# Optimization experiments

Hardware: AMD Instinct MI355X
Metric: run time of the kernel (lower is better)

The kernel has to match this reference:

```python
import jax, jax.numpy as jnp
import numpy as np

N_NODES = 100000
N_EDGES = 300000
D = 256
N_LAYERS = 4
BN_EPS = 1e-5


def setup_inputs() -> dict:
    key = jax.random.key(0)
    ks = jax.random.split(key, 6)
    x = jax.random.normal(ks[0], (N_NODES, D), dtype=jnp.float32)
    rows = jax.random.randint(ks[1], (N_EDGES,), 0, N_NODES)
    cols = jax.random.randint(ks[2], (N_EDGES,), 0, N_NODES)
    vals = jax.random.uniform(ks[3], (N_EDGES,), dtype=jnp.float32)
    stdv = 1.0 / np.sqrt(D).astype(np.float32)
    weights = jax.random.uniform(ks[4], (N_LAYERS, D, D), jnp.float32, -stdv, stdv)
    self_weights = jax.random.uniform(ks[5], (N_LAYERS, D, D), jnp.float32, -stdv, stdv)
    gammas = jnp.ones((N_LAYERS, D), jnp.float32)
    betas = jnp.zeros((N_LAYERS, D), jnp.float32)
    return {"x": x, "vals": vals, "weights": weights, "self_weights": self_weights,
            "gammas": gammas, "betas": betas, "rows": rows, "cols": cols}


def reference(x, vals, weights, self_weights, gammas, betas, rows, cols):
    n = x.shape[0]

    def gcn_layer(h, W, SW, gamma, beta):
        # support = h @ W  -> dense [N, D]
        support = h @ W
        # spmm(adj, support): out[i] = sum_{e: rows[e]==i} vals[e] * support[cols[e]]
        agg = jax.ops.segment_sum(vals[:, None] * support[cols], rows, num_segments=n)
        out = agg + h @ SW  # self-loop term (withloop=True)
        # BatchNorm1d over nodes (training-mode batch stats, biased variance)
        mean = out.mean(axis=0)
        var = out.var(axis=0)
        out = gamma * (out - mean) * jax.lax.rsqrt(var + BN_EPS) + beta
        return jax.nn.relu(out)

    h = x
    for i in range(N_LAYERS):
        h = gcn_layer(h, weights[i], self_weights[i], gammas[i], betas[i])
    # aggrmethod='concat', dense=False -> cat(final, input)
    return jnp.concatenate([h, x], axis=1)
```

## Files before the change

### kernel.cpp

```cpp
#include <hip/hip_runtime.h>
#include <hip/hip_bf16.h>
#include <stdint.h>

#define M_NODES 100000
#define NE      300000
#define D       256
#define D2      512
#define NLAYERS 4

typedef float  f32x4  __attribute__((ext_vector_type(4)));
typedef __bf16 bf16x8 __attribute__((ext_vector_type(8)));

static __device__ __forceinline__ float bf2f(uint32_t u) {
  union { uint32_t i; float f; } v; v.i = u << 16; return v.f;
}
static __device__ __forceinline__ uint32_t f2bf(float f) {
  union { float f; uint32_t i; } v; v.f = f;
  return (v.i + 0x7fffu + ((v.i >> 16) & 1u)) >> 16;
}
static __device__ __forceinline__ void gload_lds16(const void* g, void* l) {
  __builtin_amdgcn_global_load_lds((const __attribute__((address_space(1))) uint32_t*)g,
                                   (__attribute__((address_space(3))) uint32_t*)l, 16, 0, 0);
}

__global__ void hist_kernel(const int* __restrict__ rows, int* __restrict__ counts) {
  int e = blockIdx.x * 256 + threadIdx.x;
  if (e < NE) atomicAdd(&counts[rows[e]], 1);
}

__global__ void scan1_kernel(const int* __restrict__ counts, int* __restrict__ rp,
                             int* __restrict__ bsum) {
  __shared__ int sd[256];
  int tid = threadIdx.x;
  int base = blockIdx.x * 1024 + tid * 4;
  int v0 = (base + 0 < M_NODES) ? counts[base + 0] : 0;
  int v1 = (base + 1 < M_NODES) ? counts[base + 1] : 0;
  int v2 = (base + 2 < M_NODES) ? counts[base + 2] : 0;
  int v3 = (base + 3 < M_NODES) ? counts[base + 3] : 0;
  int tsum = v0 + v1 + v2 + v3;
  sd[tid] = tsum; __syncthreads();
  for (int off = 1; off < 256; off <<= 1) {
    int x = sd[tid];
    if (tid >= off) x += sd[tid - off];
    __syncthreads(); sd[tid] = x; __syncthreads();
  }
  int excl = sd[tid] - tsum;
  if (base + 0 < M_NODES) rp[base + 0] = excl; excl += v0;
  if (base + 1 < M_NODES) rp[base + 1] = excl; excl += v1;
  if (base + 2 < M_NODES) rp[base + 2] = excl; excl += v2;
  if (base + 3 < M_NODES) rp[base + 3] = excl;
  if (tid == 255) bsum[blockIdx.x] = sd[255];
}

__global__ void scan2_kernel(const int* __restrict__ bsum, int* __restrict__ boff) {
  __shared__ int sd[128];
  int tid = threadIdx.x;
  int v = (tid < 98) ? bsum[tid] : 0;
  sd[tid] = v; __syncthreads();
  for (int off = 1; off < 128; off <<= 1) {
    int x = sd[tid];
    if (tid >= off) x += sd[tid - off];
    __syncthreads(); sd[tid] = x; __syncthreads();
  }
  if (tid < 98) boff[tid] = sd[tid] - v;
}

__global__ void scan3_kernel(int* __restrict__ rp, const int* __restrict__ boff,
                             int* __restrict__ cursor) {
  int i = blockIdx.x * 256 + threadIdx.x;
  if (i > M_NODES) return;
  int v = (i < M_NODES) ? rp[i] + boff[i >> 10] : NE;
  rp[i] = v;
  if (i < M_NODES) cursor[i] = v;
}

__global__ void scatter_kernel(const int* __restrict__ rows, const int* __restrict__ cols,
                               const float* __restrict__ vals, int* __restrict__ cursor,
                               int* __restrict__ e_col, float* __restrict__ e_val) {
  int e = blockIdx.x * 256 + threadIdx.x;
  if (e >= NE) return;
  int r = rows[e];
  int p = atomicAdd(&cursor[r], 1);
  e_col[p] = cols[e];
  e_val[p] = vals[e];
}

__global__ void conv_x_kernel(const float* __restrict__ x, ushort* __restrict__ h) {
  size_t idx = (size_t)blockIdx.x * 256 + threadIdx.x;
  size_t i = idx >> 6; int c = (int)(idx & 63) * 4;
  float4 v = *(const float4*)(x + i * D + c);
  ushort4 o;
  o.x = (ushort)f2bf(v.x); o.y = (ushort)f2bf(v.y);
  o.z = (ushort)f2bf(v.z); o.w = (ushort)f2bf(v.w);
  *(ushort4*)(h + i * D + c) = o;
}

__global__ void copy_x_kernel(const float* __restrict__ x, float* __restrict__ out) {
  size_t idx = (size_t)blockIdx.x * 256 + threadIdx.x;
  size_t i = idx >> 6; int c = (int)(idx & 63) * 4;
  float4 v = *(const float4*)(x + i * D + c);
  *(float4*)(out + i * D2 + D + c) = v;
}

__global__ void conv_w_kernel(const float* __restrict__ W, const float* __restrict__ SW,
                              ushort* __restrict__ Bt) {
  int idx = blockIdx.x * 256 + threadIdx.x;
  if (idx >= NLAYERS * D2 * D) return;
  int k = idx & (D - 1);
  int n = (idx >> 8) & (D2 - 1);
  int layer = idx >> 17;
  float v = (n < D) ? W[(size_t)layer * D * D + k * D + n]
                    : SW[(size_t)layer * D * D + k * D + (n - D)];
  Bt[idx] = (ushort)f2bf(v);
}

#define BM 128
#define BN 128
#define BK 64

__global__ __launch_bounds__(256, 2)
void gemm_kernel(const ushort* __restrict__ h, const ushort* __restrict__ Bt,
                 ushort* __restrict__ outAB) {
  __shared__ __align__(16) ushort As[BM * BK];
  __shared__ __align__(16) ushort Bs[BN * BK];
  const int tid = threadIdx.x;
  const int m0 = blockIdx.x * BM;
  const int n0 = blockIdx.y * BN;
  const int wv = tid >> 6, l = tid & 63;
  const int wr = wv >> 1, wc = wv & 1;
  const int lrow = l & 15, lhi = l >> 4;

  f32x4 acc[4][4] = {};

  const int arow = tid >> 3;
  const int acb  = (tid & 7) << 4;

#pragma unroll
  for (int s = 0; s < 4; ++s) {
    const int k0 = s * BK;
#pragma unroll
    for (int p = 0; p < 4; ++p) {
      int row = p * 32 + arow;
      int grow = m0 + row; if (grow >= M_NODES) grow = M_NODES - 1;
      int gcb = acb ^ ((row & 7) << 4);
      gload_lds16(h + (size_t)grow * D + k0 + (gcb >> 1), As + row * BK + (acb >> 1));
    }
#pragma unroll
    for (int p = 0; p < 4; ++p) {
      int row = p * 32 + arow;
      int gn = n0 + row;
      int gcb = acb ^ ((row & 7) << 4);
      gload_lds16(Bt + (size_t)gn * D + k0 + (gcb >> 1), Bs + row * BK + (acb >> 1));
    }
    __syncthreads();
#pragma unroll
    for (int kk = 0; kk < 2; ++kk) {
      bf16x8 af[4], bfr[4];
#pragma unroll
      for (int mi = 0; mi < 4; ++mi) {
        int row = wr * 64 + mi * 16 + lrow;
        int off = row * 128 + ((kk * 64 + lhi * 16) ^ ((row & 7) << 4));
        af[mi] = *(const bf16x8*)((const char*)As + off);
      }
#pragma unroll
      for (int nj = 0; nj < 4; ++nj) {
        int row = wc * 64 + nj * 16 + lrow;
        int off = row * 128 + ((kk * 64 + lhi * 16) ^ ((row & 7) << 4));
        bfr[nj] = *(const bf16x8*)((const char*)Bs + off);
      }
#pragma unroll
      for (int mi = 0; mi < 4; ++mi)
#pragma unroll
        for (int nj = 0; nj < 4; ++nj)
          acc[mi][nj] = __builtin_amdgcn_mfma_f32_16x16x32_bf16(af[mi], bfr[nj], acc[mi][nj], 0, 0, 0);
    }
    __syncthreads();
  }

#pragma unroll
  for (int mi = 0; mi < 4; ++mi) {
#pragma unroll
    for (int nj = 0; nj < 4; ++nj) {
      int gc = n0 + wc * 64 + nj * 16 + lrow;
#pragma unroll
      for (int r = 0; r < 4; ++r) {
        int grow = m0 + wr * 64 + mi * 16 + lhi * 4 + r;
        if (grow < M_NODES)
          outAB[(size_t)grow * D2 + gc] = (ushort)f2bf(acc[mi][nj][r]);
      }
    }
  }
}

#define SPMM_CHUNK 16

__global__ __launch_bounds__(256, 4)
void spmm_kernel(ushort* __restrict__ AB, const int* __restrict__ rp,
                 const int* __restrict__ e_col, const float* __restrict__ e_val,
                 float* __restrict__ stats) {
  __shared__ float sstats[2 * D];
  for (int i = threadIdx.x; i < 2 * D; i += 256) sstats[i] = 0.f;
  __syncthreads();

  const int wv = threadIdx.x >> 6, l = threadIdx.x & 63;
  const int wave = blockIdx.x * 4 + wv;
  const int row0 = wave * SPMM_CHUNK;

  float s0 = 0, s1 = 0, s2 = 0, s3 = 0, q0 = 0, q1 = 0, q2 = 0, q3 = 0;

  if (row0 < M_NODES) {
    const int nrows = (M_NODES - row0 < SPMM_CHUNK) ? (M_NODES - row0) : SPMM_CHUNK;
    int myrp = (l <= nrows) ? rp[row0 + l] : 0;

    for (int t = 0; t < nrows; ++t) {
      const int i = row0 + t;
      const int e0 = __shfl(myrp, t);
      const int e1 = __shfl(myrp, t + 1);
      const int deg = e1 - e0;

      const ushort4 st = *(const ushort4*)(AB + (size_t)i * D2 + D + 4 * l);
      float a0 = bf2f(st.x), a1 = bf2f(st.y), a2 = bf2f(st.z), a3 = bf2f(st.w);

      for (int b = 0; b < deg; b += 64) {
        const int nb = (deg - b < 64) ? (deg - b) : 64;
        int   myc = (l < nb) ? e_col[e0 + b + l] : 0;
        float myv = (l < nb) ? e_val[e0 + b + l] : 0.f;

        for (int e = 0; e < nb; e += 4) {
          int cc[4]; float vv[4]; ushort4 sp[4];
#pragma unroll
          for (int j = 0; j < 4; ++j) {
            int ee = (e + j < nb) ? (e + j) : (nb - 1);
            cc[j] = __shfl(myc, ee);
            vv[j] = (e + j < nb) ? __shfl(myv, e + j) : 0.f;
            sp[j] = *(const ushort4*)(AB + (size_t)cc[j] * D2 + 4 * l);
          }
#pragma unroll
          for (int j = 0; j < 4; ++j) {
            a0 += vv[j] * bf2f(sp[j].x);
            a1 += vv[j] * bf2f(sp[j].y);
            a2 += vv[j] * bf2f(sp[j].z);
            a3 += vv[j] * bf2f(sp[j].w);
          }
        }
      }

      ushort4 o;
      o.x = (ushort)f2bf(a0); o.y = (ushort)f2bf(a1);
      o.z = (ushort)f2bf(a2); o.w = (ushort)f2bf(a3);
      *(ushort4*)(AB + (size_t)i * D2 + D + 4 * l) = o;
      s0 += a0; q0 += a0 * a0; s1 += a1; q1 += a1 * a1;
      s2 += a2; q2 += a2 * a2; s3 += a3; q3 += a3 * a3;
    }
  }

  const int c0 = 4 * l;
  atomicAdd(&sstats[c0 + 0], s0); atomicAdd(&sstats[c0 + 1], s1);
  atomicAdd(&sstats[c0 + 2], s2); atomicAdd(&sstats[c0 + 3], s3);
  atomicAdd(&sstats[D + c0 + 0], q0); atomicAdd(&sstats[D + c0 + 1], q1);
  atomicAdd(&sstats[D + c0 + 2], q2); atomicAdd(&sstats[D + c0 + 3], q3);
  __syncthreads();
  atomicAdd(&stats[threadIdx.x], sstats[threadIdx.x]);
  atomicAdd(&stats[D + threadIdx.x], sstats[D + threadIdx.x]);
}

__global__ void bn_fin_kernel(const float* __restrict__ stats, const float* __restrict__ gamma,
                              const float* __restrict__ beta, float* __restrict__ scale,
                              float* __restrict__ shift) {
  int c = threadIdx.x;
  float mean = stats[c] * (1.0f / M_NODES);
  float var = stats[D + c] * (1.0f / M_NODES) - mean * mean;
  float rstd = rsqrtf(var + 1e-5f);
  float sc = gamma[c] * rstd;
  scale[c] = sc;
  shift[c] = beta[c] - mean * sc;
}

__global__ void norm_bf16_kernel(const ushort* __restrict__ AB, const float* __restrict__ scale,
                                 const float* __restrict__ shift, ushort* __restrict__ hout) {
  size_t idx = (size_t)blockIdx.x * 256 + threadIdx.x;
  if (idx >= (size_t)M_NODES * D / 8) return;
  size_t i = idx >> 5; int c = (int)(idx & 31) * 8;
  uint4 u = *(const uint4*)(AB + i * D2 + D + c);
  float4 sc0 = *(const float4*)(scale + c), sc1 = *(const float4*)(scale + c + 4);
  float4 sh0 = *(const float4*)(shift + c), sh1 = *(const float4*)(shift + c + 4);
  float f0 = fmaxf(bf2f(u.x & 0xffff) * sc0.x + sh0.x, 0.f);
  float f1 = fmaxf(bf2f(u.x >> 16)    * sc0.y + sh0.y, 0.f);
  float f2 = fmaxf(bf2f(u.y & 0xffff) * sc0.z + sh0.z, 0.f);
  float f3 = fmaxf(bf2f(u.y >> 16)    * sc0.w + sh0.w, 0.f);
  float f4 = fmaxf(bf2f(u.z & 0xffff) * sc1.x + sh1.x, 0.f);
  float f5 = fmaxf(bf2f(u.z >> 16)    * sc1.y + sh1.y, 0.f);
  float f6 = fmaxf(bf2f(u.w & 0xffff) * sc1.z + sh1.z, 0.f);
  float f7 = fmaxf(bf2f(u.w >> 16)    * sc1.w + sh1.w, 0.f);
  uint4 o;
  o.x = f2bf(f0) | (f2bf(f1) << 16);
  o.y = f2bf(f2) | (f2bf(f3) << 16);
  o.z = f2bf(f4) | (f2bf(f5) << 16);
  o.w = f2bf(f6) | (f2bf(f7) << 16);
  *(uint4*)(hout + i * D + c) = o;
}

__global__ void norm_f32_out_kernel(const ushort* __restrict__ AB, const float* __restrict__ scale,
                                    const float* __restrict__ shift, float* __restrict__ out) {
  size_t idx = (size_t)blockIdx.x * 256 + threadIdx.x;
  if (idx >= (size_t)M_NODES * D / 8) return;
  size_t i = idx >> 5; int c = (int)(idx & 31) * 8;
  uint4 u = *(const uint4*)(AB + i * D2 + D + c);
  float4 sc0 = *(const float4*)(scale + c), sc1 = *(const float4*)(scale + c + 4);
  float4 sh0 = *(const float4*)(shift + c), sh1 = *(const float4*)(shift + c + 4);
  float4 r0, r1;
  r0.x = fmaxf(bf2f(u.x & 0xffff) * sc0.x + sh0.x, 0.f);
  r0.y = fmaxf(bf2f(u.x >> 16)    * sc0.y + sh0.y, 0.f);
  r0.z = fmaxf(bf2f(u.y & 0xffff) * sc0.z + sh0.z, 0.f);
  r0.w = fmaxf(bf2f(u.y >> 16)    * sc0.w + sh0.w, 0.f);
  r1.x = fmaxf(bf2f(u.z & 0xffff) * sc1.x + sh1.x, 0.f);
  r1.y = fmaxf(bf2f(u.z >> 16)    * sc1.y + sh1.y, 0.f);
  r1.z = fmaxf(bf2f(u.w & 0xffff) * sc1.z + sh1.z, 0.f);
  r1.w = fmaxf(bf2f(u.w >> 16)    * sc1.w + sh1.w, 0.f);
  *(float4*)(out + i * D2 + c) = r0;
  *(float4*)(out + i * D2 + c + 4) = r1;
}

extern "C" void kernel_launch(void* const* d_in, const int* in_sizes, int n_in,
                              void* d_out, int out_size, void* d_ws, size_t ws_size,
                              hipStream_t stream) {
  const float* x      = (const float*)d_in[0];
  const float* vals   = (const float*)d_in[1];
  const float* W      = (const float*)d_in[2];
  const float* SW     = (const float*)d_in[3];
  const float* gammas = (const float*)d_in[4];
  const float* betas  = (const float*)d_in[5];
  const int*   rows   = (const int*)d_in[6];
  const int*   cols   = (const int*)d_in[7];
  float* out = (float*)d_out;

  char* ws = (char*)d_ws;
  size_t off = 0;
  auto alloc = [&](size_t bytes) {
    void* p = ws + off;
    off = (off + bytes + 255) & ~(size_t)255;
    return p;
  };
  ushort* h    = (ushort*)alloc((size_t)M_NODES * D * 2);
  ushort* AB   = (ushort*)alloc((size_t)M_NODES * D2 * 2);
  ushort* Bt   = (ushort*)alloc((size_t)NLAYERS * D2 * D * 2);
  int*   rp    = (int*)alloc((M_NODES + 1) * 4);
  int*   cursor= (int*)alloc((M_NODES + 1) * 4);
  int*   e_col = (int*)alloc(NE * 4);
  float* e_val = (float*)alloc(NE * 4);
  int*   bsum  = (int*)alloc(512);
  int*   boff  = (int*)alloc(512);
  float* stats = (float*)alloc(NLAYERS * 2 * D * 4);
  float* scale = (float*)alloc(D * 4);
  float* shift = (float*)alloc(D * 4);

  hipMemsetAsync(cursor, 0, (size_t)M_NODES * 4, stream);
  hipMemsetAsync(stats, 0, (size_t)NLAYERS * 2 * D * 4, stream);

  hist_kernel<<<(NE + 255) / 256, 256, 0, stream>>>(rows, cursor);
  scan1_kernel<<<98, 256, 0, stream>>>(cursor, rp, bsum);
  scan2_kernel<<<1, 128, 0, stream>>>(bsum, boff);
  scan3_kernel<<<(M_NODES + 256) / 256, 256, 0, stream>>>(rp, boff, cursor);
  scatter_kernel<<<(NE + 255) / 256, 256, 0, stream>>>(rows, cols, vals, cursor, e_col, e_val);

  conv_x_kernel<<<(M_NODES * D / 4) / 256, 256, 0, stream>>>(x, h);
  conv_w_kernel<<<(NLAYERS * D2 * D) / 256, 256, 0, stream>>>(W, SW, Bt);
  copy_x_kernel<<<(M_NODES * D / 4) / 256, 256, 0, stream>>>(x, out);

  const int spmm_blocks = (M_NODES + SPMM_CHUNK * 4 - 1) / (SPMM_CHUNK * 4);
  for (int lyr = 0; lyr < NLAYERS; ++lyr) {
    gemm_kernel<<<dim3((M_NODES + BM - 1) / BM, D2 / BN), 256, 0, stream>>>(
        h, Bt + (size_t)lyr * D2 * D, AB);
    spmm_kernel<<<spmm_blocks, 256, 0, stream>>>(AB, rp, e_col, e_val,
                                                 stats + (size_t)lyr * 2 * D);
    bn_fin_kernel<<<1, 256, 0, stream>>>(stats + (size_t)lyr * 2 * D, gammas + lyr * D,
                                         betas + lyr * D, scale, shift);
    if (lyr < NLAYERS - 1)
      norm_bf16_kernel<<<(M_NODES * D / 8) / 256 + 1, 256, 0, stream>>>(AB, scale, shift, h);
    else
      norm_f32_out_kernel<<<(M_NODES * D / 8) / 256 + 1, 256, 0, stream>>>(AB, scale, shift, out);
  }
}
```

Baseline: 708.6 us.

## Restructure SpMM to half-wave rows with preloaded edges; fuse BN finalize into norm

The SpMM kernel now has each half-wave handle one row with 8 columns per lane and 16-byte gathers, processing two rows at once. The column and value lists for the whole 16-row chunk are preloaded into registers and broadcast with shuffles, falling back to global loads past 128 edges. The separate BN finalize kernel is folded into the normalization kernel, which recomputes scale and shift per thread, and the x-to-bf16 conversion and output copy of x are merged into one kernel. This cuts kernel launches and per-edge load latency, at the cost of divergence when the two rows paired in a wave differ in degree.

```diff
diff --git a/kernel.cpp b/kernel.cpp
--- a/kernel.cpp
+++ b/kernel.cpp
@@ -85,21 +85,16 @@
   e_val[p] = vals[e];
 }
 
-__global__ void conv_x_kernel(const float* __restrict__ x, ushort* __restrict__ h) {
+__global__ void prep_x_kernel(const float* __restrict__ x, ushort* __restrict__ h,
+                              float* __restrict__ out) {
   size_t idx = (size_t)blockIdx.x * 256 + threadIdx.x;
   size_t i = idx >> 6; int c = (int)(idx & 63) * 4;
   float4 v = *(const float4*)(x + i * D + c);
+  *(float4*)(out + i * D2 + D + c) = v;
   ushort4 o;
   o.x = (ushort)f2bf(v.x); o.y = (ushort)f2bf(v.y);
   o.z = (ushort)f2bf(v.z); o.w = (ushort)f2bf(v.w);
   *(ushort4*)(h + i * D + c) = o;
-}
-
-__global__ void copy_x_kernel(const float* __restrict__ x, float* __restrict__ out) {
-  size_t idx = (size_t)blockIdx.x * 256 + threadIdx.x;
-  size_t i = idx >> 6; int c = (int)(idx & 63) * 4;
-  float4 v = *(const float4*)(x + i * D + c);
-  *(float4*)(out + i * D2 + D + c) = v;
 }
 
 __global__ void conv_w_kernel(const float* __restrict__ W, const float* __restrict__ SW,
@@ -203,122 +198,141 @@
   __syncthreads();
 
   const int wv = threadIdx.x >> 6, l = threadIdx.x & 63;
+  const int hl = l >> 5, lc = l & 31;
   const int wave = blockIdx.x * 4 + wv;
   const int row0 = wave * SPMM_CHUNK;
 
-  float s0 = 0, s1 = 0, s2 = 0, s3 = 0, q0 = 0, q1 = 0, q2 = 0, q3 = 0;
+  float s[8] = {}, q[8] = {};
 
   if (row0 < M_NODES) {
-    const int nrows = (M_NODES - row0 < SPMM_CHUNK) ? (M_NODES - row0) : SPMM_CHUNK;
-    int myrp = (l <= nrows) ? rp[row0 + l] : 0;
-
-    for (int t = 0; t < nrows; ++t) {
-      const int i = row0 + t;
-      const int e0 = __shfl(myrp, t);
-      const int e1 = __shfl(myrp, t + 1);
-      const int deg = e1 - e0;
-
-      const ushort4 st = *(const ushort4*)(AB + (size_t)i * D2 + D + 4 * l);
-      float a0 = bf2f(st.x), a1 = bf2f(st.y), a2 = bf2f(st.z), a3 = bf2f(st.w);
-
-      for (int b = 0; b < deg; b += 64) {
-        const int nb = (deg - b < 64) ? (deg - b) : 64;
-        int   myc = (l < nb) ? e_col[e0 + b + l] : 0;
-        float myv = (l < nb) ? e_val[e0 + b + l] : 0.f;
-
-        for (int e = 0; e < nb; e += 4) {
-          int cc[4]; float vv[4]; ushort4 sp[4];
-#pragma unroll
-          for (int j = 0; j < 4; ++j) {
-            int ee = (e + j < nb) ? (e + j) : (nb - 1);
-            cc[j] = __shfl(myc, ee);
-            vv[j] = (e + j < nb) ? __shfl(myv, e + j) : 0.f;
-            sp[j] = *(const ushort4*)(AB + (size_t)cc[j] * D2 + 4 * l);
+    int myrp = (l <= SPMM_CHUNK) ? rp[row0 + l] : 0;
+    const int ebase = __shfl(myrp, 0);
+    const int ecnt  = __shfl(myrp, SPMM_CHUNK) - ebase;
+    int   myc0 = (l < ecnt)      ? e_col[ebase + l]      : 0;
+    float myv0 = (l < ecnt)      ? e_val[ebase + l]      : 0.f;
+    int   myc1 = (64 + l < ecnt) ? e_col[ebase + 64 + l] : 0;
+    float myv1 = (64 + l < ecnt) ? e_val[ebase + 64 + l] : 0.f;
+
+    for (int t = 0; t < SPMM_CHUNK; t += 2) {
+      const int i = row0 + t + hl;
+      const int eA0 = __shfl(myrp, t);
+      const int eA1 = __shfl(myrp, t + 1);
+      const int eB1 = __shfl(myrp, t + 2);
+      const int d0 = eA1 - eA0, d1 = eB1 - eA1;
+      const int e0  = hl ? eA1 : eA0;
+      const int deg = hl ? d1  : d0;
+      const int degmax = (d0 > d1) ? d0 : d1;
+
+      float a[8] = {};
+
+      for (int b = 0; b < degmax; b += 4) {
+        float vv[4]; uint4 sp[4];
+#pragma unroll
+        for (int j = 0; j < 4; ++j) {
+          int ej = b + j;
+          int ecl = (ej < deg) ? ej : ((deg > 0) ? deg - 1 : 0);
+          int slot = e0 - ebase + ecl;
+          int sl = slot & 63;
+          int cA = __shfl(myc0, sl);
+          int cB = __shfl(myc1, sl);
+          float vA = __shfl(myv0, sl);
+          float vB = __shfl(myv1, sl);
+          int   c = (slot < 64) ? cA : cB;
+          float v = (slot < 64) ? vA : vB;
+          if (slot >= 128 && ej < deg) {
+            c = e_col[e0 + ecl]; v = e_val[e0 + ecl];
           }
-#pragma unroll
-          for (int j = 0; j < 4; ++j) {
-            a0 += vv[j] * bf2f(sp[j].x);
-            a1 += vv[j] * bf2f(sp[j].y);
-            a2 += vv[j] * bf2f(sp[j].z);
-            a3 += vv[j] * bf2f(sp[j].w);
-          }
+          vv[j] = (ej < deg) ? v : 0.f;
+          sp[j] = *(const uint4*)(AB + (size_t)c * D2 + lc * 8);
+        }
+#pragma unroll
+        for (int j = 0; j < 4; ++j) {
+          a[0] += vv[j] * bf2f(sp[j].x & 0xffff);
+          a[1] += vv[j] * bf2f(sp[j].x >> 16);
+          a[2] += vv[j] * bf2f(sp[j].y & 0xffff);
+          a[3] += vv[j] * bf2f(sp[j].y >> 16);
+          a[4] += vv[j] * bf2f(sp[j].z & 0xffff);
+          a[5] += vv[j] * bf2f(sp[j].z >> 16);
+          a[6] += vv[j] * bf2f(sp[j].w & 0xffff);
+          a[7] += vv[j] * bf2f(sp[j].w >> 16);
         }
       }
 
-      ushort4 o;
-      o.x = (ushort)f2bf(a0); o.y = (ushort)f2bf(a1);
-      o.z = (ushort)f2bf(a2); o.w = (ushort)f2bf(a3);
-      *(ushort4*)(AB + (size_t)i * D2 + D + 4 * l) = o;
-      s0 += a0; q0 += a0 * a0; s1 += a1; q1 += a1 * a1;
-      s2 += a2; q2 += a2 * a2; s3 += a3; q3 += a3 * a3;
-    }
-  }
-
-  const int c0 = 4 * l;
-  atomicAdd(&sstats[c0 + 0], s0); atomicAdd(&sstats[c0 + 1], s1);
-  atomicAdd(&sstats[c0 + 2], s2); atomicAdd(&sstats[c0 + 3], s3);
-  atomicAdd(&sstats[D + c0 + 0], q0); atomicAdd(&sstats[D + c0 + 1], q1);
-  atomicAdd(&sstats[D + c0 + 2], q2); atomicAdd(&sstats[D + c0 + 3], q3);
+      const uint4 st = *(const uint4*)(AB + (size_t)i * D2 + D + lc * 8);
+      a[0] += bf2f(st.x & 0xffff); a[1] += bf2f(st.x >> 16);
+      a[2] += bf2f(st.y & 0xffff); a[3] += bf2f(st.y >> 16);
+      a[4] += bf2f(st.z & 0xffff); a[5] += bf2f(st.z >> 16);
+      a[6] += bf2f(st.w & 0xffff); a[7] += bf2f(st.w >> 16);
+
+      uint4 o;
+      o.x = f2bf(a[0]) | (f2bf(a[1]) << 16);
+      o.y = f2bf(a[2]) | (f2bf(a[3]) << 16);
+      o.z = f2bf(a[4]) | (f2bf(a[5]) << 16);
+      o.w = f2bf(a[6]) | (f2bf(a[7]) << 16);
+      *(uint4*)(AB + (size_t)i * D2 + D + lc * 8) = o;
+
+#pragma unroll
+      for (int k = 0; k < 8; ++k) { s[k] += a[k]; q[k] += a[k] * a[k]; }
+    }
+  }
+
+  const int c0 = lc * 8;
+#pragma unroll
+  for (int k = 0; k < 8; ++k) {
+    atomicAdd(&sstats[c0 + k], s[k]);
+    atomicAdd(&sstats[D + c0 + k], q[k]);
+  }
   __syncthreads();
   atomicAdd(&stats[threadIdx.x], sstats[threadIdx.x]);
   atomicAdd(&stats[D + threadIdx.x], sstats[D + threadIdx.x]);
 }
 
-__global__ void bn_fin_kernel(const float* __restrict__ stats, const float* __restrict__ gamma,
-                              const float* __restrict__ beta, float* __restrict__ scale,
-                              float* __restrict__ shift) {
-  int c = threadIdx.x;
-  float mean = stats[c] * (1.0f / M_NODES);
-  float var = stats[D + c] * (1.0f / M_NODES) - mean * mean;
-  float rstd = rsqrtf(var + 1e-5f);
-  float sc = gamma[c] * rstd;
-  scale[c] = sc;
-  shift[c] = beta[c] - mean * sc;
-}
-
-__global__ void norm_bf16_kernel(const ushort* __restrict__ AB, const float* __restrict__ scale,
-                                 const float* __restrict__ shift, ushort* __restrict__ hout) {
-  size_t idx = (size_t)blockIdx.x * 256 + threadIdx.x;
-  if (idx >= (size_t)M_NODES * D / 8) return;
-  size_t i = idx >> 5; int c = (int)(idx & 31) * 8;
-  uint4 u = *(const uint4*)(AB + i * D2 + D + c);
-  float4 sc0 = *(const float4*)(scale + c), sc1 = *(const float4*)(scale + c + 4);
-  float4 sh0 = *(const float4*)(shift + c), sh1 = *(const float4*)(shift + c + 4);
-  float f0 = fmaxf(bf2f(u.x & 0xffff) * sc0.x + sh0.x, 0.f);
-  float f1 = fmaxf(bf2f(u.x >> 16)    * sc0.y + sh0.y, 0.f);
-  float f2 = fmaxf(bf2f(u.y & 0xffff) * sc0.z + sh0.z, 0.f);
-  float f3 = fmaxf(bf2f(u.y >> 16)    * sc0.w + sh0.w, 0.f);
-  float f4 = fmaxf(bf2f(u.z & 0xffff) * sc1.x + sh1.x, 0.f);
-  float f5 = fmaxf(bf2f(u.z >> 16)    * sc1.y + sh1.y, 0.f);
-  float f6 = fmaxf(bf2f(u.w & 0xffff) * sc1.z + sh1.z, 0.f);
-  float f7 = fmaxf(bf2f(u.w >> 16)    * sc1.w + sh1.w, 0.f);
-  uint4 o;
-  o.x = f2bf(f0) | (f2bf(f1) << 16);
-  o.y = f2bf(f2) | (f2bf(f3) << 16);
-  o.z = f2bf(f4) | (f2bf(f5) << 16);
-  o.w = f2bf(f6) | (f2bf(f7) << 16);
-  *(uint4*)(hout + i * D + c) = o;
-}
-
-__global__ void norm_f32_out_kernel(const ushort* __restrict__ AB, const float* __restrict__ scale,
-                                    const float* __restrict__ shift, float* __restrict__ out) {
-  size_t idx = (size_t)blockIdx.x * 256 + threadIdx.x;
-  if (idx >= (size_t)M_NODES * D / 8) return;
-  size_t i = idx >> 5; int c = (int)(idx & 31) * 8;
-  uint4 u = *(const uint4*)(AB + i * D2 + D + c);
-  float4 sc0 = *(const float4*)(scale + c), sc1 = *(const float4*)(scale + c + 4);
-  float4 sh0 = *(const float4*)(shift + c), sh1 = *(const float4*)(shift + c + 4);
-  float4 r0, r1;
-  r0.x = fmaxf(bf2f(u.x & 0xffff) * sc0.x + sh0.x, 0.f);
-  r0.y = fmaxf(bf2f(u.x >> 16)    * sc0.y + sh0.y, 0.f);
-  r0.z = fmaxf(bf2f(u.y & 0xffff) * sc0.z + sh0.z, 0.f);
-  r0.w = fmaxf(bf2f(u.y >> 16)    * sc0.w + sh0.w, 0.f);
-  r1.x = fmaxf(bf2f(u.z & 0xffff) * sc1.x + sh1.x, 0.f);
-  r1.y = fmaxf(bf2f(u.z >> 16)    * sc1.y + sh1.y, 0.f);
-  r1.z = fmaxf(bf2f(u.w & 0xffff) * sc1.z + sh1.z, 0.f);
-  r1.w = fmaxf(bf2f(u.w >> 16)    * sc1.w + sh1.w, 0.f);
-  *(float4*)(out + i * D2 + c) = r0;
-  *(float4*)(out + i * D2 + c + 4) = r1;
+template<bool LAST>
+__global__ void norm_kernel(const ushort* __restrict__ AB, const float* __restrict__ stats,
+                            const float* __restrict__ gamma, const float* __restrict__ beta,
+                            ushort* __restrict__ hout, float* __restrict__ out) {
+  const int cs = threadIdx.x & 31;
+  const int rr = threadIdx.x >> 5;
+  const int c0 = cs * 8;
+
+  float sc[8], sh[8];
+#pragma unroll
+  for (int k = 0; k < 8; ++k) {
+    float mean = stats[c0 + k] * (1.0f / M_NODES);
+    float var  = stats[D + c0 + k] * (1.0f / M_NODES) - mean * mean;
+    float rstd = rsqrtf(var + 1e-5f);
+    float g = gamma[c0 + k];
+    sc[k] = g * rstd;
+    sh[k] = beta[c0 + k] - mean * sc[k];
+  }
+
+  const int r0 = blockIdx.x * 64;
+#pragma unroll
+  for (int rb = 0; rb < 8; ++rb) {
+    int r = r0 + rb * 8 + rr;
+    if (r >= M_NODES) break;
+    const uint4 u = *(const uint4*)(AB + (size_t)r * D2 + D + c0);
+    float f[8];
+    f[0] = bf2f(u.x & 0xffff); f[1] = bf2f(u.x >> 16);
+    f[2] = bf2f(u.y & 0xffff); f[3] = bf2f(u.y >> 16);
+    f[4] = bf2f(u.z & 0xffff); f[5] = bf2f(u.z >> 16);
+    f[6] = bf2f(u.w & 0xffff); f[7] = bf2f(u.w >> 16);
+#pragma unroll
+    for (int k = 0; k < 8; ++k) f[k] = fmaxf(f[k] * sc[k] + sh[k], 0.f);
+    if (LAST) {
+      float4 r0v = { f[0], f[1], f[2], f[3] };
+      float4 r1v = { f[4], f[5], f[6], f[7] };
+      *(float4*)(out + (size_t)r * D2 + c0) = r0v;
+      *(float4*)(out + (size_t)r * D2 + c0 + 4) = r1v;
+    } else {
+      uint4 o;
+      o.x = f2bf(f[0]) | (f2bf(f[1]) << 16);
+      o.y = f2bf(f[2]) | (f2bf(f[3]) << 16);
+      o.z = f2bf(f[4]) | (f2bf(f[5]) << 16);
+      o.w = f2bf(f[6]) | (f2bf(f[7]) << 16);
+      *(uint4*)(hout + (size_t)r * D + c0) = o;
+    }
+  }
 }
 
 extern "C" void kernel_launch(void* const* d_in, const int* in_sizes, int n_in,
@@ -351,8 +365,6 @@
   int*   bsum  = (int*)alloc(512);
   int*   boff  = (int*)alloc(512);
   float* stats = (float*)alloc(NLAYERS * 2 * D * 4);
-  float* scale = (float*)alloc(D * 4);
-  float* shift = (float*)alloc(D * 4);
 
   hipMemsetAsync(cursor, 0, (size_t)M_NODES * 4, stream);
   hipMemsetAsync(stats, 0, (size_t)NLAYERS * 2 * D * 4, stream);
@@ -363,21 +375,21 @@
   scan3_kernel<<<(M_NODES + 256) / 256, 256, 0, stream>>>(rp, boff, cursor);
   scatter_kernel<<<(NE + 255) / 256, 256, 0, stream>>>(rows, cols, vals, cursor, e_col, e_val);
 
-  conv_x_kernel<<<(M_NODES * D / 4) / 256, 256, 0, stream>>>(x, h);
+  prep_x_kernel<<<(M_NODES * D / 4) / 256, 256, 0, stream>>>(x, h, out);
   conv_w_kernel<<<(NLAYERS * D2 * D) / 256, 256, 0, stream>>>(W, SW, Bt);
-  copy_x_kernel<<<(M_NODES * D / 4) / 256, 256, 0, stream>>>(x, out);
 
   const int spmm_blocks = (M_NODES + SPMM_CHUNK * 4 - 1) / (SPMM_CHUNK * 4);
+  const int norm_blocks = (M_NODES + 63) / 64;
   for (int lyr = 0; lyr < NLAYERS; ++lyr) {
     gemm_kernel<<<dim3((M_NODES + BM - 1) / BM, D2 / BN), 256, 0, stream>>>(
         h, Bt + (size_t)lyr * D2 * D, AB);
     spmm_kernel<<<spmm_blocks, 256, 0, stream>>>(AB, rp, e_col, e_val,
                                                  stats + (size_t)lyr * 2 * D);
-    bn_fin_kernel<<<1, 256, 0, stream>>>(stats + (size_t)lyr * 2 * D, gammas + lyr * D,
-                                         betas + lyr * D, scale, shift);
     if (lyr < NLAYERS - 1)
-      norm_bf16_kernel<<<(M_NODES * D / 8) / 256 + 1, 256, 0, stream>>>(AB, scale, shift, h);
+      norm_kernel<false><<<norm_blocks, 256, 0, stream>>>(
+          AB, stats + (size_t)lyr * 2 * D, gammas + lyr * D, betas + lyr * D, h, nullptr);
     else
-      norm_f32_out_kernel<<<(M_NODES * D / 8) / 256 + 1, 256, 0, stream>>>(AB, scale, shift, out);
-  }
-}
+      norm_kernel<true><<<norm_blocks, 256, 0, stream>>>(
+          AB, stats + (size_t)lyr * 2 * D, gammas + lyr * D, betas + lyr * D, nullptr, out);
+  }
+}
```

Measured after the change: 717.5 us. No clear change (+1.3%).
